# Performance work log

Hardware: AMD Instinct MI355X
Metric: run time of the kernel (lower is better)

## Reference

```python
import jax, jax.numpy as jnp
import numpy as np

D = 512   # dense write dimension
M = 64    # number of experts
B = 16    # per-expert sparse code width
N = 8192  # tokens
K = 4     # experts per token (top-k)


def _normalize_U(U):
    # UnitColNormPadded(dim=1): each column of the (D+1, b) expert matrix
    # is rescaled to unit L2 norm along the padded (D+1) axis.
    nrm = jnp.sqrt(jnp.sum(U * U, axis=1, keepdims=True))
    return U / nrm


def setup_inputs() -> dict:
    key = jax.random.key(0)
    k1, k2, k3 = jax.random.split(key, 3)
    h_sparse = jax.random.normal(k1, (N, K, B), dtype=jnp.float32)
    topk_idxs = jax.random.randint(k2, (N, K), 0, M)
    U = jax.random.normal(k3, (M, D + 1, B), dtype=jnp.float32)
    return {"h_sparse": h_sparse, "topk_idxs": topk_idxs, "U": U}


def reference(h_sparse, topk_idxs, U):
    Un = _normalize_U(U)                      # (m, D+1, b)
    U_active = Un[topk_idxs][:, :, :D, :]     # gather -> (N, k, D, b)
    writes = jnp.einsum('nkdb,nkb->nd', U_active, h_sparse)   # (N, D)
    h_recon = jnp.einsum('nkdb,nd->nkb', U_active, writes)    # (N, k, b)
    h_target = jax.lax.stop_gradient(h_sparse)
    diff = h_recon - h_target
    writer_aux_loss = jnp.mean(diff * diff)
    return writes, writer_aux_loss
```

## Files before the change

kernel.cpp:

```cpp
#include <hip/hip_runtime.h>

#define DD 512
#define MM 64
#define BB 16
#define NN 8192
#define KK 4
#define DP1 513
#define CAP 1024
#define GPE 8
#define NPAIR (NN * KK)

#define CNT_B  0
#define BKT_B  256
#define U_B    131328
#define UT_B   1179904
#define PART_B 2228480
#define WS_NEED (PART_B + (size_t)2 * KK * NN * DD)

typedef unsigned int uint;
typedef unsigned short ushort;
typedef __attribute__((ext_vector_type(8))) short short8;
typedef __attribute__((ext_vector_type(4))) float f32x4;

struct __align__(8) U16x4 { ushort x, y, z, w; };

__device__ __forceinline__ ushort f2bf(float f) {
    uint u = __builtin_bit_cast(uint, f);
    uint r = (u + 0x7FFFu + ((u >> 16) & 1u)) >> 16;
    return (ushort)r;
}
__device__ __forceinline__ float bf2f(ushort s) {
    return __builtin_bit_cast(float, (uint)s << 16);
}

__global__ __launch_bounds__(256) void prep_kernel(
    const float* __restrict__ U, void* __restrict__ ws,
    float* __restrict__ loss_slot)
{
    const int m = blockIdx.x, t = threadIdx.x;
    const float* Um = U + (long)m * DP1 * BB;
    __shared__ float red[256];
    __shared__ float inv_s[BB];

    float a = 0.f;
    for (int i = t; i < DP1 * BB; i += 256) { float v = Um[i]; a += v * v; }
    red[t] = a;
    __syncthreads();
    if (t < BB) {
        float tot = 0.f;
        #pragma unroll
        for (int j = 0; j < 16; ++j) tot += red[t + 16 * j];
        inv_s[t] = rsqrtf(tot);
    }
    __syncthreads();

    ushort* ub = (ushort*)((char*)ws + U_B) + (long)m * DD * BB;
    ushort* ut = (ushort*)((char*)ws + UT_B) + (long)m * BB * DD;

    for (int i = t; i < DD * BB / 2; i += 256) {
        const int e0 = 2 * i;
        const float2 v = *(const float2*)(Um + e0);
        const int b0 = e0 & 15;
        const uint pk = (uint)f2bf(v.x * inv_s[b0]) |
                        ((uint)f2bf(v.y * inv_s[b0 + 1]) << 16);
        *(uint*)(ub + e0) = pk;
    }
    {
        const int b = t & 15, dg = t >> 4;
        const float iv = inv_s[b];
        for (int dd = 0; dd < 32; dd += 2) {
            const int d = dg * 32 + dd;
            const uint pk = (uint)f2bf(Um[(long)d * BB + b] * iv) |
                            ((uint)f2bf(Um[(long)(d + 1) * BB + b] * iv) << 16);
            *(uint*)(ut + (long)b * DD + d) = pk;
        }
    }
    if (m == 0 && t == 0) *loss_slot = 0.f;
}

__global__ __launch_bounds__(256) void build_buckets(
    const int* __restrict__ topk, void* __restrict__ ws)
{
    int* cnt = (int*)ws;
    ushort* bkt = (ushort*)((char*)ws + BKT_B);
    __shared__ int lc[MM], lb[MM];
    const int t = threadIdx.x;
    if (t < MM) lc[t] = 0;
    __syncthreads();
    const int p = blockIdx.x * 256 + t;
    const int e = topk[p];
    const int my = atomicAdd(&lc[e], 1);
    __syncthreads();
    if (t < MM) lb[t] = atomicAdd(&cnt[t], lc[t]);
    __syncthreads();
    bkt[e * CAP + lb[e] + my] = (ushort)p;
}

__global__ __launch_bounds__(256) void pass_writes_mfma(
    const float* __restrict__ h_sparse, void* __restrict__ ws)
{
    const int e = blockIdx.x >> 3, g = blockIdx.x & 7;
    const int wave = threadIdx.x >> 6, lane = threadIdx.x & 63;
    const int quad = lane >> 4, l15 = lane & 15;

    const int* cnt = (const int*)ws;
    const ushort* bkt = (const ushort*)((const char*)ws + BKT_B);
    const ushort* Ue = (const ushort*)((const char*)ws + U_B) + (long)e * DD * BB;
    ushort* part = (ushort*)((char*)ws + PART_B);

    const int c  = cnt[e];
    const int lo = (c * g) >> 3;
    const int hi = (c * (g + 1)) >> 3;

    for (int base = lo + wave * 16; base < hi; base += 64) {
        const int pidx = base + l15;
        const bool valid = pidx < hi;
        const int id = valid ? (int)bkt[e * CAP + pidx] : 0;
        const int n = id >> 2, k = id & 3;

        short8 bfrag = (short8)0;
        if (quad < 2 && valid) {
            const float4* hp = (const float4*)(h_sparse + (long)id * BB + quad * 8);
            const float4 h0 = hp[0], h1 = hp[1];
            bfrag[0] = (short)f2bf(h0.x); bfrag[1] = (short)f2bf(h0.y);
            bfrag[2] = (short)f2bf(h0.z); bfrag[3] = (short)f2bf(h0.w);
            bfrag[4] = (short)f2bf(h1.x); bfrag[5] = (short)f2bf(h1.y);
            bfrag[6] = (short)f2bf(h1.z); bfrag[7] = (short)f2bf(h1.w);
        }
        ushort* prow = part + ((long)(k * NN + n) << 9);

        #pragma unroll 4
        for (int dt = 0; dt < 32; ++dt) {
            short8 afrag = (short8)0;
            if (quad < 2)
                afrag = *(const short8*)(Ue + ((long)(dt * 16 + l15) << 4) + quad * 8);
            f32x4 acc = {0.f, 0.f, 0.f, 0.f};
            acc = __builtin_amdgcn_mfma_f32_16x16x32_bf16(afrag, bfrag, acc, 0, 0, 0);
            if (valid) {
                U16x4 st;
                st.x = f2bf(acc[0]); st.y = f2bf(acc[1]);
                st.z = f2bf(acc[2]); st.w = f2bf(acc[3]);
                *(U16x4*)(prow + dt * 16 + quad * 4) = st;
            }
        }
    }
}

__global__ __launch_bounds__(256) void pass_recon_mfma(
    const float* __restrict__ h_sparse, void* __restrict__ ws,
    float* __restrict__ out)
{
    const int e = blockIdx.x >> 3, g = blockIdx.x & 7;
    const int wave = threadIdx.x >> 6, lane = threadIdx.x & 63;
    const int quad = lane >> 4, l15 = lane & 15;
    const int t = threadIdx.x;

    const int* cnt = (const int*)ws;
    const ushort* bkt = (const ushort*)((const char*)ws + BKT_B);
    const ushort* Ute = (const ushort*)((const char*)ws + UT_B) + (long)e * BB * DD;
    const ushort* part = (const ushort*)((const char*)ws + PART_B);

    __shared__ float loss_blk;
    if (t == 0) loss_blk = 0.f;
    __syncthreads();

    const int c  = cnt[e];
    const int lo = (c * g) >> 3;
    const int hi = (c * (g + 1)) >> 3;

    float lsum = 0.f;

    for (int base = lo + wave * 16; base < hi; base += 64) {
        const int pidx = base + l15;
        const bool valid = pidx < hi;
        const int id = valid ? (int)bkt[e * CAP + pidx] : 0;
        const int n = id >> 2, k = id & 3;
        const ushort* p0 = part + ((long)n << 9);
        float* outrow = out + (long)n * DD;
        const bool writer = valid && (k == 0);

        f32x4 acc = {0.f, 0.f, 0.f, 0.f};

        #pragma unroll 4
        for (int kk = 0; kk < 16; ++kk) {
            const int doff = kk * 32 + quad * 8;
            const short8 s0 = *(const short8*)(p0 + doff);
            const short8 s1 = *(const short8*)(p0 + (long)NN * DD + doff);
            const short8 s2 = *(const short8*)(p0 + 2L * NN * DD + doff);
            const short8 s3 = *(const short8*)(p0 + 3L * NN * DD + doff);
            float w[8];
            short8 afrag;
            #pragma unroll
            for (int j = 0; j < 8; ++j) {
                w[j] = bf2f((ushort)s0[j]) + bf2f((ushort)s1[j]) +
                       bf2f((ushort)s2[j]) + bf2f((ushort)s3[j]);
                afrag[j] = (short)f2bf(w[j]);
            }
            if (writer) {
                *(float4*)(outrow + doff)     = make_float4(w[0], w[1], w[2], w[3]);
                *(float4*)(outrow + doff + 4) = make_float4(w[4], w[5], w[6], w[7]);
            }
            const short8 bfrag = *(const short8*)(Ute + (long)l15 * DD + doff);
            acc = __builtin_amdgcn_mfma_f32_16x16x32_bf16(afrag, bfrag, acc, 0, 0, 0);
        }

        #pragma unroll
        for (int r = 0; r < 4; ++r) {
            const int pr = base + quad * 4 + r;
            if (pr < hi) {
                const int id2 = (int)bkt[e * CAP + pr];
                const float h = h_sparse[(long)id2 * BB + l15];
                const float d = acc[r] - h;
                lsum += d * d;
            }
        }
    }

    #pragma unroll
    for (int off = 32; off > 0; off >>= 1) lsum += __shfl_xor(lsum, off, 64);
    if (lane == 0 && lsum != 0.f) atomicAdd(&loss_blk, lsum);
    __syncthreads();
    if (t == 0 && loss_blk != 0.f)
        atomicAdd(out + (long)NN * DD, loss_blk * (1.0f / ((float)NN * KK * BB)));
}

__global__ __launch_bounds__(256) void norm_kernel(
    const float* __restrict__ U, float* __restrict__ inv_norm,
    float* __restrict__ loss_slot)
{
    const int m = blockIdx.x;
    const int t = threadIdx.x;
    const float* Um = U + (long)m * DP1 * BB;
    float acc = 0.f;
    for (int idx = t; idx < DP1 * BB; idx += 256) {
        float v = Um[idx];
        acc += v * v;
    }
    __shared__ float s[256];
    s[t] = acc;
    __syncthreads();
    if (t < BB) {
        float tot = 0.f;
        #pragma unroll
        for (int j = 0; j < 16; ++j) tot += s[t + 16 * j];
        inv_norm[m * BB + t] = rsqrtf(tot);
    }
    if (m == 0 && t == 0) *loss_slot = 0.f;
}

__global__ __launch_bounds__(256) void dense_write_kernel(
    const float* __restrict__ h_sparse,
    const int*   __restrict__ topk,
    const float* __restrict__ U,
    const float* __restrict__ inv_norm,
    float* __restrict__ out)
{
    const int n = blockIdx.x;
    const int t = threadIdx.x;

    __shared__ float hs[KK * BB];
    __shared__ float ho[KK * BB];
    __shared__ float inv_s[KK * BB];
    __shared__ int   eidx[KK];
    __shared__ float w_s[DD];
    __shared__ float red[256];

    if (t < KK) eidx[t] = topk[n * KK + t];
    __syncthreads();
    if (t < KK * BB) {
        const int k = t / BB, b = t % BB;
        const float h  = h_sparse[(long)n * KK * BB + t];
        const float iv = inv_norm[eidx[k] * BB + b];
        ho[t]    = h;
        inv_s[t] = iv;
        hs[t]    = h * iv;
    }
    __syncthreads();

    #pragma unroll
    for (int dd = 0; dd < 2; ++dd) {
        const int d = t + dd * 256;
        float w = 0.f;
        #pragma unroll
        for (int k = 0; k < KK; ++k) {
            const float4* row = (const float4*)(U + ((long)eidx[k] * DP1 + d) * BB);
            #pragma unroll
            for (int q = 0; q < 4; ++q) {
                const float4 u4 = row[q];
                w += u4.x * hs[k * BB + 4 * q + 0];
                w += u4.y * hs[k * BB + 4 * q + 1];
                w += u4.z * hs[k * BB + 4 * q + 2];
                w += u4.w * hs[k * BB + 4 * q + 3];
            }
        }
        w_s[d] = w;
        out[(long)n * DD + d] = w;
    }
    __syncthreads();

    {
        const int pair = t & 63;
        const int k = pair >> 4, b = pair & 15;
        const int ch = t >> 6;
        const float* Ucol = U + (long)eidx[k] * DP1 * BB + b;
        float p = 0.f;
        #pragma unroll 8
        for (int d = ch * 128; d < ch * 128 + 128; ++d) {
            p += Ucol[(long)d * BB] * w_s[d];
        }
        red[t] = p;
    }
    __syncthreads();

    if (t < 64) {
        const float recon = (red[t] + red[t + 64] + red[t + 128] + red[t + 192]) * inv_s[t];
        const float diff  = recon - ho[t];
        float sq = diff * diff;
        #pragma unroll
        for (int off = 32; off > 0; off >>= 1) sq += __shfl_down(sq, off, 64);
        if (t == 0) {
            atomicAdd(out + (long)NN * DD, sq * (1.0f / ((float)NN * KK * BB)));
        }
    }
}


extern "C" void kernel_launch(void* const* d_in, const int* in_sizes, int n_in,
                              void* d_out, int out_size, void* d_ws, size_t ws_size,
                              hipStream_t stream) {
    const float* h_sparse = (const float*)d_in[0];
    const int*   topk     = (const int*)d_in[1];
    const float* U        = (const float*)d_in[2];
    float* out = (float*)d_out;

    if (ws_size >= WS_NEED) {
        hipMemsetAsync(d_ws, 0, 256, stream);
        hipLaunchKernelGGL(prep_kernel, dim3(MM), dim3(256), 0, stream,
                           U, d_ws, out + (long)NN * DD);
        hipLaunchKernelGGL(build_buckets, dim3(NPAIR / 256), dim3(256), 0, stream,
                           topk, d_ws);
        hipLaunchKernelGGL(pass_writes_mfma, dim3(MM * GPE), dim3(256), 0, stream,
                           h_sparse, d_ws);
        hipLaunchKernelGGL(pass_recon_mfma, dim3(MM * GPE), dim3(256), 0, stream,
                           h_sparse, d_ws, out);
    } else {
        float* inv_norm = (float*)d_ws;
        hipLaunchKernelGGL(norm_kernel, dim3(MM), dim3(256), 0, stream,
                           U, inv_norm, out + (long)NN * DD);
        hipLaunchKernelGGL(dense_write_kernel, dim3(NN), dim3(256), 0, stream,
                           h_sparse, topk, U, inv_norm, out);
    }
}
```

Before: 141.5 us.

## Split U prep into norm and pack kernels; add separate writes reduction pass

Splits the per-expert prep into a norm kernel and a 256-block pack kernel that transposes through shared memory, replacing the strided transposed stores. The four-way bf16 partial sum is moved out of the recon pass into a dedicated reduce_w kernel, which writes the fp32 outputs once plus a bf16 copy of writes. The recon pass then reads that single bf16 buffer instead of four partial buffers per pair. This removes redundant 4x partial reads for every (token, expert) pair, at the cost of two extra launches and a larger workspace.

```diff
diff --git a/kernel.cpp b/kernel.cpp
--- a/kernel.cpp
+++ b/kernel.cpp
@@ -12,10 +12,12 @@
 
 #define CNT_B  0
 #define BKT_B  256
-#define U_B    131328
-#define UT_B   1179904
-#define PART_B 2228480
-#define WS_NEED (PART_B + (size_t)2 * KK * NN * DD)
+#define INV_B  131328
+#define U_B    135424
+#define UT_B   1184000
+#define WBF_B  2232576
+#define PART_B 10621184
+#define WS_NEED 44175616
 
 typedef unsigned int uint;
 typedef unsigned short ushort;
@@ -33,49 +35,64 @@
     return __builtin_bit_cast(float, (uint)s << 16);
 }
 
-__global__ __launch_bounds__(256) void prep_kernel(
-    const float* __restrict__ U, void* __restrict__ ws,
+__global__ __launch_bounds__(256) void norm_kernel(
+    const float* __restrict__ U, float* __restrict__ inv_norm,
     float* __restrict__ loss_slot)
 {
     const int m = blockIdx.x, t = threadIdx.x;
     const float* Um = U + (long)m * DP1 * BB;
-    __shared__ float red[256];
-    __shared__ float inv_s[BB];
-
-    float a = 0.f;
-    for (int i = t; i < DP1 * BB; i += 256) { float v = Um[i]; a += v * v; }
-    red[t] = a;
+    float acc = 0.f;
+    for (int idx = t; idx < DP1 * BB; idx += 256) {
+        float v = Um[idx];
+        acc += v * v;
+    }
+    __shared__ float s[256];
+    s[t] = acc;
     __syncthreads();
     if (t < BB) {
         float tot = 0.f;
         #pragma unroll
-        for (int j = 0; j < 16; ++j) tot += red[t + 16 * j];
-        inv_s[t] = rsqrtf(tot);
-    }
-    __syncthreads();
-
-    ushort* ub = (ushort*)((char*)ws + U_B) + (long)m * DD * BB;
-    ushort* ut = (ushort*)((char*)ws + UT_B) + (long)m * BB * DD;
-
-    for (int i = t; i < DD * BB / 2; i += 256) {
+        for (int j = 0; j < 16; ++j) tot += s[t + 16 * j];
+        inv_norm[m * BB + t] = rsqrtf(tot);
+    }
+    if (m == 0 && t == 0) *loss_slot = 0.f;
+}
+
+__global__ __launch_bounds__(256) void pack_kernel(
+    const float* __restrict__ U, void* __restrict__ ws)
+{
+    const int m = blockIdx.x >> 2, sl = blockIdx.x & 3;
+    const int t = threadIdx.x;
+    const float* Um = U + (long)m * DP1 * BB + (long)sl * 128 * BB;
+    const float* invp = (const float*)((const char*)ws + INV_B) + m * BB;
+    ushort* ub = (ushort*)((char*)ws + U_B) + (long)m * DD * BB + sl * 128 * BB;
+    ushort* ut = (ushort*)((char*)ws + UT_B) + (long)m * BB * DD + sl * 128;
+
+    __shared__ float inv_s[BB];
+    __shared__ ushort tr[BB][136];
+
+    if (t < BB) inv_s[t] = invp[t];
+    __syncthreads();
+
+    #pragma unroll
+    for (int iter = 0; iter < 4; ++iter) {
+        const int i = t + iter * 256;
         const int e0 = 2 * i;
+        const int dl = e0 >> 4, b0 = e0 & 15;
         const float2 v = *(const float2*)(Um + e0);
-        const int b0 = e0 & 15;
-        const uint pk = (uint)f2bf(v.x * inv_s[b0]) |
-                        ((uint)f2bf(v.y * inv_s[b0 + 1]) << 16);
-        *(uint*)(ub + e0) = pk;
-    }
+        const ushort bv0 = f2bf(v.x * inv_s[b0]);
+        const ushort bv1 = f2bf(v.y * inv_s[b0 + 1]);
+        *(uint*)(ub + e0) = (uint)bv0 | ((uint)bv1 << 16);
+        tr[b0][dl] = bv0;
+        tr[b0 + 1][dl] = bv1;
+    }
+    __syncthreads();
+
     {
-        const int b = t & 15, dg = t >> 4;
-        const float iv = inv_s[b];
-        for (int dd = 0; dd < 32; dd += 2) {
-            const int d = dg * 32 + dd;
-            const uint pk = (uint)f2bf(Um[(long)d * BB + b] * iv) |
-                            ((uint)f2bf(Um[(long)(d + 1) * BB + b] * iv) << 16);
-            *(uint*)(ut + (long)b * DD + d) = pk;
-        }
-    }
-    if (m == 0 && t == 0) *loss_slot = 0.f;
+        const int b = t >> 4, doff = (t & 15) * 8;
+        const uint4 val = *(const uint4*)&tr[b][doff];
+        *(uint4*)(ut + (long)b * DD + doff) = val;
+    }
 }
 
 __global__ __launch_bounds__(256) void build_buckets(
@@ -146,6 +163,41 @@
     }
 }
 
+__global__ __launch_bounds__(256) void reduce_w(
+    void* __restrict__ ws, float* __restrict__ out)
+{
+    const uint4* part4 = (const uint4*)((const char*)ws + PART_B);
+    uint4* wbf4 = (uint4*)((char*)ws + WBF_B);
+    const int gsz = NN * DD / 8;
+    const int gid = blockIdx.x * 256 + threadIdx.x;
+
+    const uint4 v0 = part4[gid];
+    const uint4 v1 = part4[(long)gsz + gid];
+    const uint4 v2 = part4[2L * gsz + gid];
+    const uint4 v3 = part4[3L * gsz + gid];
+
+    float s[8];
+    s[0] = bf2f((ushort)v0.x) + bf2f((ushort)v1.x) + bf2f((ushort)v2.x) + bf2f((ushort)v3.x);
+    s[1] = bf2f((ushort)(v0.x >> 16)) + bf2f((ushort)(v1.x >> 16)) + bf2f((ushort)(v2.x >> 16)) + bf2f((ushort)(v3.x >> 16));
+    s[2] = bf2f((ushort)v0.y) + bf2f((ushort)v1.y) + bf2f((ushort)v2.y) + bf2f((ushort)v3.y);
+    s[3] = bf2f((ushort)(v0.y >> 16)) + bf2f((ushort)(v1.y >> 16)) + bf2f((ushort)(v2.y >> 16)) + bf2f((ushort)(v3.y >> 16));
+    s[4] = bf2f((ushort)v0.z) + bf2f((ushort)v1.z) + bf2f((ushort)v2.z) + bf2f((ushort)v3.z);
+    s[5] = bf2f((ushort)(v0.z >> 16)) + bf2f((ushort)(v1.z >> 16)) + bf2f((ushort)(v2.z >> 16)) + bf2f((ushort)(v3.z >> 16));
+    s[6] = bf2f((ushort)v0.w) + bf2f((ushort)v1.w) + bf2f((ushort)v2.w) + bf2f((ushort)v3.w);
+    s[7] = bf2f((ushort)(v0.w >> 16)) + bf2f((ushort)(v1.w >> 16)) + bf2f((ushort)(v2.w >> 16)) + bf2f((ushort)(v3.w >> 16));
+
+    float4* out4 = (float4*)out;
+    out4[(long)gid * 2 + 0] = make_float4(s[0], s[1], s[2], s[3]);
+    out4[(long)gid * 2 + 1] = make_float4(s[4], s[5], s[6], s[7]);
+
+    uint4 pk;
+    pk.x = (uint)f2bf(s[0]) | ((uint)f2bf(s[1]) << 16);
+    pk.y = (uint)f2bf(s[2]) | ((uint)f2bf(s[3]) << 16);
+    pk.z = (uint)f2bf(s[4]) | ((uint)f2bf(s[5]) << 16);
+    pk.w = (uint)f2bf(s[6]) | ((uint)f2bf(s[7]) << 16);
+    wbf4[gid] = pk;
+}
+
 __global__ __launch_bounds__(256) void pass_recon_mfma(
     const float* __restrict__ h_sparse, void* __restrict__ ws,
     float* __restrict__ out)
@@ -158,7 +210,7 @@
     const int* cnt = (const int*)ws;
     const ushort* bkt = (const ushort*)((const char*)ws + BKT_B);
     const ushort* Ute = (const ushort*)((const char*)ws + UT_B) + (long)e * BB * DD;
-    const ushort* part = (const ushort*)((const char*)ws + PART_B);
+    const ushort* wbf = (const ushort*)((const char*)ws + WBF_B);
 
     __shared__ float loss_blk;
     if (t == 0) loss_blk = 0.f;
@@ -174,32 +226,15 @@
         const int pidx = base + l15;
         const bool valid = pidx < hi;
         const int id = valid ? (int)bkt[e * CAP + pidx] : 0;
-        const int n = id >> 2, k = id & 3;
-        const ushort* p0 = part + ((long)n << 9);
-        float* outrow = out + (long)n * DD;
-        const bool writer = valid && (k == 0);
+        const int n = id >> 2;
+        const ushort* wrow = wbf + ((long)n << 9);
 
         f32x4 acc = {0.f, 0.f, 0.f, 0.f};
 
         #pragma unroll 4
         for (int kk = 0; kk < 16; ++kk) {
             const int doff = kk * 32 + quad * 8;
-            const short8 s0 = *(const short8*)(p0 + doff);
-            const short8 s1 = *(const short8*)(p0 + (long)NN * DD + doff);
-            const short8 s2 = *(const short8*)(p0 + 2L * NN * DD + doff);
-            const short8 s3 = *(const short8*)(p0 + 3L * NN * DD + doff);
-            float w[8];
-            short8 afrag;
-            #pragma unroll
-            for (int j = 0; j < 8; ++j) {
-                w[j] = bf2f((ushort)s0[j]) + bf2f((ushort)s1[j]) +
-                       bf2f((ushort)s2[j]) + bf2f((ushort)s3[j]);
-                afrag[j] = (short)f2bf(w[j]);
-            }
-            if (writer) {
-                *(float4*)(outrow + doff)     = make_float4(w[0], w[1], w[2], w[3]);
-                *(float4*)(outrow + doff + 4) = make_float4(w[4], w[5], w[6], w[7]);
-            }
+            const short8 afrag = *(const short8*)(wrow + doff);
             const short8 bfrag = *(const short8*)(Ute + (long)l15 * DD + doff);
             acc = __builtin_amdgcn_mfma_f32_16x16x32_bf16(afrag, bfrag, acc, 0, 0, 0);
         }
@@ -222,30 +257,6 @@
     __syncthreads();
     if (t == 0 && loss_blk != 0.f)
         atomicAdd(out + (long)NN * DD, loss_blk * (1.0f / ((float)NN * KK * BB)));
-}
-
-__global__ __launch_bounds__(256) void norm_kernel(
-    const float* __restrict__ U, float* __restrict__ inv_norm,
-    float* __restrict__ loss_slot)
-{
-    const int m = blockIdx.x;
-    const int t = threadIdx.x;
-    const float* Um = U + (long)m * DP1 * BB;
-    float acc = 0.f;
-    for (int idx = t; idx < DP1 * BB; idx += 256) {
-        float v = Um[idx];
-        acc += v * v;
-    }
-    __shared__ float s[256];
-    s[t] = acc;
-    __syncthreads();
-    if (t < BB) {
-        float tot = 0.f;
-        #pragma unroll
-        for (int j = 0; j < 16; ++j) tot += s[t + 16 * j];
-        inv_norm[m * BB + t] = rsqrtf(tot);
-    }
-    if (m == 0 && t == 0) *loss_slot = 0.f;
 }
 
 __global__ __launch_bounds__(256) void dense_write_kernel(
@@ -333,14 +344,18 @@
     const float* U        = (const float*)d_in[2];
     float* out = (float*)d_out;
 
-    if (ws_size >= WS_NEED) {
+    if (ws_size >= (size_t)WS_NEED) {
         hipMemsetAsync(d_ws, 0, 256, stream);
-        hipLaunchKernelGGL(prep_kernel, dim3(MM), dim3(256), 0, stream,
-                           U, d_ws, out + (long)NN * DD);
+        hipLaunchKernelGGL(norm_kernel, dim3(MM), dim3(256), 0, stream,
+                           U, (float*)((char*)d_ws + INV_B), out + (long)NN * DD);
+        hipLaunchKernelGGL(pack_kernel, dim3(MM * 4), dim3(256), 0, stream,
+                           U, d_ws);
         hipLaunchKernelGGL(build_buckets, dim3(NPAIR / 256), dim3(256), 0, stream,
                            topk, d_ws);
         hipLaunchKernelGGL(pass_writes_mfma, dim3(MM * GPE), dim3(256), 0, stream,
                            h_sparse, d_ws);
+        hipLaunchKernelGGL(reduce_w, dim3(NN * DD / 8 / 256), dim3(256), 0, stream,
+                           d_ws, out);
         hipLaunchKernelGGL(pass_recon_mfma, dim3(MM * GPE), dim3(256), 0, stream,
                            h_sparse, d_ws, out);
     } else {
```

Result: faster. 136.7 us (-3.4%).
